# Kernel tuning notes

Measured on AMD Instinct MI355X. Metric: run time of the kernel, lower is better.

## Reference

```python
import jax, jax.numpy as jnp
import numpy as np

N_NODES = 100000
NEG_SLOPE = 0.2
EPS = 1e-16


def gat_conv(x, src, dst, W, a_src, a_dst, b):
    # x: [N, in], W: [in, d]. PyG GATConv with heads=1, concat -> [N, d]
    h = x @ W                                   # [N, d]
    e = jax.nn.leaky_relu((h @ a_src)[src] + (h @ a_dst)[dst], NEG_SLOPE)  # [E]
    # softmax over incoming edges per destination node
    m = jax.ops.segment_max(e, dst, num_segments=N_NODES)   # [N]
    m = jnp.where(jnp.isfinite(m), m, 0.0)
    ex = jnp.exp(e - m[dst])                                 # [E]
    denom = jax.ops.segment_sum(ex, dst, num_segments=N_NODES)
    alpha = ex / (denom[dst] + EPS)                          # [E]
    out = jax.ops.segment_sum(alpha[:, None] * h[src], dst, num_segments=N_NODES)
    return out + b


def setup_inputs() -> dict:
    key = jax.random.key(0)
    ks = jax.random.split(key, 12)
    d_in, d_h = 64, 64
    x = jax.random.normal(ks[0], (N_NODES, d_in), dtype=jnp.float32)
    edge_index = jax.random.randint(ks[1], (2, 1200000), 0, N_NODES, dtype=jnp.int32)
    s = 1.0 / np.sqrt(d_in)
    return {
        "x": x,
        "edge_index": edge_index,
        "W1": jax.random.normal(ks[2], (d_in, d_h), dtype=jnp.float32) * s,
        "a_src1": jax.random.normal(ks[3], (d_h,), dtype=jnp.float32) * s,
        "a_dst1": jax.random.normal(ks[4], (d_h,), dtype=jnp.float32) * s,
        "b1": jnp.zeros((d_h,), dtype=jnp.float32),
        "W2": jax.random.normal(ks[5], (d_h, d_h), dtype=jnp.float32) * s,
        "a_src2": jax.random.normal(ks[6], (d_h,), dtype=jnp.float32) * s,
        "a_dst2": jax.random.normal(ks[7], (d_h,), dtype=jnp.float32) * s,
        "b2": jnp.zeros((d_h,), dtype=jnp.float32),
        "W_out": jax.random.normal(ks[8], (d_h, 1), dtype=jnp.float32) * s,
        "b_out": jnp.zeros((1,), dtype=jnp.float32),
    }


def reference(x, edge_index, W1, a_src1, a_dst1, b1, W2, a_src2, a_dst2, b2, W_out, b_out):
    # PyG GATConv adds self-loops by default
    loop = jnp.arange(N_NODES, dtype=edge_index.dtype)
    src = jnp.concatenate([edge_index[0], loop])
    dst = jnp.concatenate([edge_index[1], loop])
    h = jax.nn.relu(gat_conv(x, src, dst, W1, a_src1, a_dst1, b1))
    h = jax.nn.relu(gat_conv(h, src, dst, W2, a_src2, a_dst2, b2))
    g = jnp.mean(h, axis=0, keepdims=True)   # [1, d]
    return g @ W_out + b_out                  # [1, 1]
```

## Files before the change

kernel.cpp:

```cpp
#include <hip/hip_runtime.h>
#include <math.h>

#define NEG_SLOPE 0.2f
#define EPS 1e-16f
#define PPART 256
#define BMAX 512
#define BSTRIDE 6144
#define GAGG_BLOCKS 2048

__device__ __forceinline__ unsigned short f2bf(float f) {
    unsigned int x = __float_as_uint(f);
    unsigned int r = (x + 0x7FFFu + ((x >> 16) & 1u)) >> 16;
    return (unsigned short)r;
}
__device__ __forceinline__ float bf2f(unsigned short u) {
    return __uint_as_float(((unsigned int)u) << 16);
}

#define XPAD 132
__global__ __launch_bounds__(256) void gemm_hs(
    const float* __restrict__ X, const float* __restrict__ W,
    const float* __restrict__ asrc, const float* __restrict__ adst,
    unsigned short* __restrict__ Hb, float* __restrict__ Ss, float* __restrict__ Sd, int N)
{
    __shared__ float Ws[64 * 64];
    __shared__ float Xs[64 * XPAD];
    int t = threadIdx.x;
    int row0 = blockIdx.x * 128;

    {
        const float4* W4 = (const float4*)W;
        float4* Ws4 = (float4*)Ws;
#pragma unroll
        for (int i = 0; i < 4; ++i) Ws4[i * 256 + t] = W4[i * 256 + t];
    }
    {
        const float4* X4 = (const float4*)X;
#pragma unroll
        for (int i = 0; i < 8; ++i) {
            int v = i * 256 + t;
            int r = v >> 4;
            int c4 = (v & 15) * 4;
            int grow = row0 + r;
            float4 xv = make_float4(0.f, 0.f, 0.f, 0.f);
            if (grow < N) xv = X4[(size_t)grow * 16 + (c4 >> 2)];
            Xs[(c4 + 0) * XPAD + r] = xv.x;
            Xs[(c4 + 1) * XPAD + r] = xv.y;
            Xs[(c4 + 2) * XPAD + r] = xv.z;
            Xs[(c4 + 3) * XPAD + r] = xv.w;
        }
    }
    __syncthreads();

    int cg = t & 7;
    int rg = t >> 3;
    float acc[4][8] = {{0.f}};

#pragma unroll 8
    for (int k = 0; k < 64; ++k) {
        float4 xv = *(const float4*)&Xs[k * XPAD + rg * 4];
        float4 w0 = *(const float4*)&Ws[k * 64 + cg * 8];
        float4 w1 = *(const float4*)&Ws[k * 64 + cg * 8 + 4];
        float xr[4] = {xv.x, xv.y, xv.z, xv.w};
        float wc[8] = {w0.x, w0.y, w0.z, w0.w, w1.x, w1.y, w1.z, w1.w};
#pragma unroll
        for (int r = 0; r < 4; ++r)
#pragma unroll
            for (int c = 0; c < 8; ++c)
                acc[r][c] = fmaf(xr[r], wc[c], acc[r][c]);
    }

    float a_s[8], a_d[8];
#pragma unroll
    for (int j = 0; j < 8; ++j) { a_s[j] = asrc[cg * 8 + j]; a_d[j] = adst[cg * 8 + j]; }
#pragma unroll
    for (int r = 0; r < 4; ++r) {
        int row = row0 + rg * 4 + r;
        float s1 = 0.f, s2 = 0.f;
#pragma unroll
        for (int j = 0; j < 8; ++j) {
            s1 = fmaf(acc[r][j], a_s[j], s1);
            s2 = fmaf(acc[r][j], a_d[j], s2);
        }
#pragma unroll
        for (int off = 1; off < 8; off <<= 1) {
            s1 += __shfl_xor(s1, off);
            s2 += __shfl_xor(s2, off);
        }
        if (row < N) {
            unsigned int p0 = (unsigned int)f2bf(acc[r][0]) | ((unsigned int)f2bf(acc[r][1]) << 16);
            unsigned int p1 = (unsigned int)f2bf(acc[r][2]) | ((unsigned int)f2bf(acc[r][3]) << 16);
            unsigned int p2 = (unsigned int)f2bf(acc[r][4]) | ((unsigned int)f2bf(acc[r][5]) << 16);
            unsigned int p3 = (unsigned int)f2bf(acc[r][6]) | ((unsigned int)f2bf(acc[r][7]) << 16);
            *(uint4*)&Hb[(size_t)row * 64 + cg * 8] = make_uint4(p0, p1, p2, p3);
            if (cg == 0) { Ss[row] = s1; Sd[row] = s2; }
        }
    }
}

__global__ __launch_bounds__(256) void bucket_scatter(
    const int* __restrict__ src, const int* __restrict__ dst,
    int E0, int N, int B, int per,
    int* __restrict__ gcur, int* __restrict__ part)
{
    __shared__ int lh[BMAX];
    __shared__ int gb[BMAX];
    __shared__ int lcur[BMAX];
    int t = threadIdx.x, b = blockIdx.x;
    for (int i = t; i < BMAX; i += 256) lh[i] = 0;
    __syncthreads();
    int Etot = E0 + N;
    int i0 = b * per, i1 = min(Etot, i0 + per);
    for (int i = i0 + t; i < i1; i += 256) {
        int d = (i < E0) ? dst[i] : (i - E0);
        atomicAdd(&lh[d >> 8], 1);
    }
    __syncthreads();
    for (int bin = t; bin < B; bin += 256) {
        int c = lh[bin];
        gb[bin] = c ? atomicAdd(&gcur[bin], c) : 0;
        lcur[bin] = 0;
    }
    __syncthreads();
    for (int i = i0 + t; i < i1; i += 256) {
        int s, d;
        if (i < E0) { s = src[i]; d = dst[i]; } else { s = d = i - E0; }
        int bin = d >> 8;
        int off = atomicAdd(&lcur[bin], 1);
        part[bin * BSTRIDE + gb[bin] + off] = ((d & 255) << 24) | s;
    }
}

__global__ __launch_bounds__(256) void bucket_sort(
    const int* __restrict__ gcur, const int* __restrict__ part,
    int* __restrict__ ptr, int* __restrict__ csr_src,
    int4* __restrict__ smallL, int4* __restrict__ bigL,
    int* __restrict__ nSmall, int* __restrict__ nBig,
    int N, int B, int Etot)
{
    __shared__ int cnts[256];
    __shared__ int sh[256];
    __shared__ int cur[256];
    __shared__ int sBase, bBase, sCnt, bCnt;
    int t = threadIdx.x, bkt = blockIdx.x;

    int v = 0;
    for (int i = t; i < bkt; i += 256) v += gcur[i];
    sh[t] = v;
    __syncthreads();
    for (int off = 128; off; off >>= 1) {
        if (t < off) sh[t] += sh[t + off];
        __syncthreads();
    }
    int base = sh[0];
    int myCnt = gcur[bkt];
    __syncthreads();

    cnts[t] = 0;
    if (t == 0) { sCnt = 0; bCnt = 0; }
    __syncthreads();
    int pbase = bkt * BSTRIDE;
    for (int i = t; i < myCnt; i += 256)
        atomicAdd(&cnts[((unsigned)part[pbase + i]) >> 24], 1);
    __syncthreads();
    sh[t] = cnts[t];
    __syncthreads();
    for (int off = 1; off < 256; off <<= 1) {
        int x = (t >= off) ? sh[t - off] : 0;
        __syncthreads();
        sh[t] += x;
        __syncthreads();
    }
    int lptr = (t > 0) ? sh[t - 1] : 0;
    int node = bkt * 256 + t;
    int deg = cnts[t];
    int p0 = base + lptr;
    if (node < N) ptr[node] = p0;
    if (bkt == 0 && t == 0) ptr[N] = Etot;
    cur[t] = lptr;
    __syncthreads();
    for (int i = t; i < myCnt; i += 256) {
        int p = part[pbase + i];
        int local = ((unsigned)p) >> 24;
        int s = p & 0xFFFFFF;
        int pos = atomicAdd(&cur[local], 1);
        csr_src[base + pos] = s;
    }

    bool isSm = (node < N) && (deg <= 16);
    bool isBg = (node < N) && (deg > 16);
    int myPos = -1;
    if (isSm) myPos = atomicAdd(&sCnt, 1);
    if (isBg) myPos = atomicAdd(&bCnt, 1);
    __syncthreads();
    if (t == 0) {
        sBase = atomicAdd(nSmall, sCnt);
        bBase = atomicAdd(nBig, bCnt);
    }
    __syncthreads();
    if (isSm) smallL[sBase + myPos] = make_int4(node, p0, deg, 0);
    if (isBg) bigL[bBase + myPos] = make_int4(node, p0, deg, 0);
}

__global__ __launch_bounds__(256) void gat_agg_small(
    const int4* __restrict__ lst, const int* __restrict__ nSmallP,
    const int* __restrict__ csr_src,
    const float* __restrict__ Ss, const float* __restrict__ Sd,
    const unsigned short* __restrict__ Hb, const float* __restrict__ bias,
    float* __restrict__ A)
{
    int w = (blockIdx.x * blockDim.x + threadIdx.x) >> 6;
    int lane = threadIdx.x & 63;
    int g = lane >> 4;
    int il = lane & 15;
    int gb = lane & 48;
    int nS = *nSmallP;
    int totWaves = (gridDim.x * blockDim.x) >> 6;
    const ushort4* H4 = (const ushort4*)Hb;
    float4 bv = ((const float4*)bias)[il];

    for (int slot0 = w * 4; slot0 < nS; slot0 += totWaves * 4) {
        int slot = slot0 + g;
        int node = -1, p0 = 0, deg = 0;
        if (slot < nS) { int4 e = lst[slot]; node = e.x; p0 = e.y; deg = e.z; }
        float sdv = (node >= 0) ? Sd[node] : 0.f;
        int s = 0; float e = -INFINITY;
        if (il < deg) {
            s = csr_src[p0 + il];
            float v = Ss[s] + sdv;
            e = (v > 0.f) ? v : NEG_SLOPE * v;
        }
        float m = e;
#pragma unroll
        for (int off = 8; off; off >>= 1) m = fmaxf(m, __shfl_xor(m, off));
        float ex = (il < deg) ? __expf(e - m) : 0.f;
        float den = ex;
#pragma unroll
        for (int off = 8; off; off >>= 1) den += __shfl_xor(den, off);
        float inv = 1.f / (den + EPS);

        float4 acc = make_float4(0.f, 0.f, 0.f, 0.f);
        for (int j = 0; j < deg; ++j) {
            int   sj = __shfl(s, gb + j);
            float aj = __shfl(ex, gb + j);
            ushort4 hv = H4[(size_t)sj * 16 + il];
            acc.x = fmaf(aj, bf2f(hv.x), acc.x);
            acc.y = fmaf(aj, bf2f(hv.y), acc.y);
            acc.z = fmaf(aj, bf2f(hv.z), acc.z);
            acc.w = fmaf(aj, bf2f(hv.w), acc.w);
        }
        if (node >= 0) {
            float4 o;
            o.x = fmaf(acc.x, inv, bv.x); o.x = (o.x > 0.f) ? o.x : 0.f;
            o.y = fmaf(acc.y, inv, bv.y); o.y = (o.y > 0.f) ? o.y : 0.f;
            o.z = fmaf(acc.z, inv, bv.z); o.z = (o.z > 0.f) ? o.z : 0.f;
            o.w = fmaf(acc.w, inv, bv.w); o.w = (o.w > 0.f) ? o.w : 0.f;
            ((float4*)A)[(size_t)node * 16 + il] = o;
        }
    }
}

__global__ __launch_bounds__(256) void gat_agg_big(
    const int4* __restrict__ lst, const int* __restrict__ nBigP,
    const int* __restrict__ csr_src,
    const float* __restrict__ Ss, const float* __restrict__ Sd,
    const unsigned short* __restrict__ Hb, const float* __restrict__ bias,
    float* __restrict__ A)
{
    int w = (blockIdx.x * blockDim.x + threadIdx.x) >> 6;
    int lane = threadIdx.x & 63;
    int nB = *nBigP;
    int totWaves = (gridDim.x * blockDim.x) >> 6;
    int q  = lane >> 4;
    int fl = lane & 15;
    const ushort4* H4 = (const ushort4*)Hb;

    for (int slot = w; slot < nB; slot += totWaves) {
        int4 ent = lst[slot];
        int node = ent.x, p0 = ent.y, deg = ent.z;
        float sdv = Sd[node];
        float4 acc = make_float4(0.f, 0.f, 0.f, 0.f);
        float inv;

        if (deg <= 64) {
            int s = 0; float e = -INFINITY;
            if (lane < deg) {
                s = csr_src[p0 + lane];
                float v = Ss[s] + sdv;
                e = (v > 0.f) ? v : NEG_SLOPE * v;
            }
            float m = e;
#pragma unroll
            for (int off = 32; off; off >>= 1) m = fmaxf(m, __shfl_xor(m, off));
            float ex = (lane < deg) ? __expf(e - m) : 0.f;
            float den = ex;
#pragma unroll
            for (int off = 32; off; off >>= 1) den += __shfl_xor(den, off);
            inv = 1.f / (den + EPS);
            for (int jb = 0; jb < deg; jb += 4) {
                int j = jb + q;
                int   sj = __shfl(s, j);
                float aj = __shfl(ex, j);
                ushort4 hv = H4[(size_t)sj * 16 + fl];
                acc.x = fmaf(aj, bf2f(hv.x), acc.x);
                acc.y = fmaf(aj, bf2f(hv.y), acc.y);
                acc.z = fmaf(aj, bf2f(hv.z), acc.z);
                acc.w = fmaf(aj, bf2f(hv.w), acc.w);
            }
        } else {
            float m = -INFINITY;
            for (int base = 0; base < deg; base += 64) {
                int idx = base + lane;
                float e = -INFINITY;
                if (idx < deg) {
                    int s = csr_src[p0 + idx];
                    float v = Ss[s] + sdv;
                    e = (v > 0.f) ? v : NEG_SLOPE * v;
                }
#pragma unroll
                for (int off = 32; off; off >>= 1) e = fmaxf(e, __shfl_xor(e, off));
                m = fmaxf(m, e);
            }
            float den = 0.f;
            for (int base = 0; base < deg; base += 64) {
                int idx = base + lane;
                float ex = 0.f;
                if (idx < deg) {
                    int s = csr_src[p0 + idx];
                    float v = Ss[s] + sdv;
                    float e = (v > 0.f) ? v : NEG_SLOPE * v;
                    ex = __expf(e - m);
                }
#pragma unroll
                for (int off = 32; off; off >>= 1) ex += __shfl_xor(ex, off);
                den += ex;
            }
            inv = 1.f / (den + EPS);
            for (int base = 0; base < deg; base += 64) {
                int idx = base + lane;
                int s = 0; float ex = 0.f;
                if (idx < deg) {
                    s = csr_src[p0 + idx];
                    float v = Ss[s] + sdv;
                    float e = (v > 0.f) ? v : NEG_SLOPE * v;
                    ex = __expf(e - m);
                }
                int cnt = min(64, deg - base);
                for (int jb = 0; jb < cnt; jb += 4) {
                    int j = jb + q;
                    int   sj = __shfl(s, j);
                    float aj = __shfl(ex, j);
                    ushort4 hv = H4[(size_t)sj * 16 + fl];
                    acc.x = fmaf(aj, bf2f(hv.x), acc.x);
                    acc.y = fmaf(aj, bf2f(hv.y), acc.y);
                    acc.z = fmaf(aj, bf2f(hv.z), acc.z);
                    acc.w = fmaf(aj, bf2f(hv.w), acc.w);
                }
            }
        }

#pragma unroll
        for (int off = 16; off < 64; off <<= 1) {
            acc.x += __shfl_xor(acc.x, off);
            acc.y += __shfl_xor(acc.y, off);
            acc.z += __shfl_xor(acc.z, off);
            acc.w += __shfl_xor(acc.w, off);
        }
        if (q == 0) {
            float4 bv = ((const float4*)bias)[fl];
            float4 o;
            o.x = fmaf(acc.x, inv, bv.x); o.x = (o.x > 0.f) ? o.x : 0.f;
            o.y = fmaf(acc.y, inv, bv.y); o.y = (o.y > 0.f) ? o.y : 0.f;
            o.z = fmaf(acc.z, inv, bv.z); o.z = (o.z > 0.f) ? o.z : 0.f;
            o.w = fmaf(acc.w, inv, bv.w); o.w = (o.w > 0.f) ? o.w : 0.f;
            ((float4*)A)[(size_t)node * 16 + fl] = o;
        }
    }
}

__global__ __launch_bounds__(256) void colsum(const float* __restrict__ A, int total,
                                              float* __restrict__ G)
{
    __shared__ float red[256];
    int t = threadIdx.x;
    int idx = blockIdx.x * blockDim.x + t;
    int stride = gridDim.x * blockDim.x;
    float acc = 0.f;
    for (int i = idx; i < total; i += stride) acc += A[i];
    red[t] = acc;
    __syncthreads();
    if (t < 64) {
        float s = red[t] + red[t + 64] + red[t + 128] + red[t + 192];
        unsafeAtomicAdd(&G[t], s);
    }
}

__global__ void final_out(const float* __restrict__ G, const float* __restrict__ Wout,
                          const float* __restrict__ bout, float* __restrict__ out, float invN)
{
    int lane = threadIdx.x;
    float v = G[lane] * invN * Wout[lane];
#pragma unroll
    for (int off = 32; off; off >>= 1) v += __shfl_down(v, off);
    if (lane == 0) out[0] = v + bout[0];
}

extern "C" void kernel_launch(void* const* d_in, const int* in_sizes, int n_in,
                              void* d_out, int out_size, void* d_ws, size_t ws_size,
                              hipStream_t stream)
{
    const float* x    = (const float*)d_in[0];
    const int*   ei   = (const int*)d_in[1];
    const float* W1   = (const float*)d_in[2];
    const float* as1  = (const float*)d_in[3];
    const float* ad1  = (const float*)d_in[4];
    const float* b1   = (const float*)d_in[5];
    const float* W2   = (const float*)d_in[6];
    const float* as2  = (const float*)d_in[7];
    const float* ad2  = (const float*)d_in[8];
    const float* b2   = (const float*)d_in[9];
    const float* Wout = (const float*)d_in[10];
    const float* bout = (const float*)d_in[11];
    float* out = (float*)d_out;

    int N    = in_sizes[0] / 64;
    int E0   = in_sizes[1] / 2;
    int Etot = E0 + N;
    const int* srcp = ei;
    const int* dstp = ei + E0;

    int B   = (N + 255) >> 8;
    int per = (Etot + PPART - 1) / PPART;

    unsigned short* Hb = (unsigned short*)d_ws;
    float* A   = (float*)d_ws + (size_t)N * 32;
    float* Ss  = A + (size_t)N * 64;
    float* Sd  = Ss + N;
    float* G   = Sd + N;
    int* ptr   = (int*)(G + 64);
    int* gcur  = ptr + N + 1;
    int* nSmall = gcur + 512;
    int* nBig   = nSmall + 1;
    int* part  = nBig + 1;
    int* csr_src = part + (size_t)B * BSTRIDE;
    int4* smallL = (int4*)(csr_src + Etot);
    int4* bigL   = smallL + N;

    int gGemm = (N + 127) / 128;

    hipMemsetAsync(gcur, 0, (512 + 2) * sizeof(int), stream);
    bucket_scatter<<<PPART, 256, 0, stream>>>(srcp, dstp, E0, N, B, per, gcur, part);
    bucket_sort<<<B, 256, 0, stream>>>(gcur, part, ptr, csr_src, smallL, bigL,
                                       nSmall, nBig, N, B, Etot);

    gemm_hs<<<gGemm, 256, 0, stream>>>(x, W1, as1, ad1, Hb, Ss, Sd, N);
    gat_agg_small<<<GAGG_BLOCKS, 256, 0, stream>>>(smallL, nSmall, csr_src, Ss, Sd, Hb, b1, A);
    gat_agg_big<<<GAGG_BLOCKS, 256, 0, stream>>>(bigL, nBig, csr_src, Ss, Sd, Hb, b1, A);

    gemm_hs<<<gGemm, 256, 0, stream>>>(A, W2, as2, ad2, Hb, Ss, Sd, N);
    gat_agg_small<<<GAGG_BLOCKS, 256, 0, stream>>>(smallL, nSmall, csr_src, Ss, Sd, Hb, b2, A);
    gat_agg_big<<<GAGG_BLOCKS, 256, 0, stream>>>(bigL, nBig, csr_src, Ss, Sd, Hb, b2, A);

    hipMemsetAsync(G, 0, 64 * 4, stream);
    colsum<<<304, 256, 0, stream>>>(A, N * 64, G);
    final_out<<<1, 64, 0, stream>>>(G, Wout, bout, out, 1.0f / (float)N);
}
```

Before: 287.5 us.

## Fuse scatter with first GEMM, merge aggregation kernels, fold readout into layer-2

After: 236.8 us. -17.6%, faster.

```diff
diff --git a/kernel.cpp b/kernel.cpp
--- a/kernel.cpp
+++ b/kernel.cpp
@@ -18,15 +18,15 @@
 }
 
 #define XPAD 132
-__global__ __launch_bounds__(256) void gemm_hs(
+__device__ __forceinline__ void gemm_body(
+    char* smem, int bid, int t,
     const float* __restrict__ X, const float* __restrict__ W,
     const float* __restrict__ asrc, const float* __restrict__ adst,
     unsigned short* __restrict__ Hb, float* __restrict__ Ss, float* __restrict__ Sd, int N)
 {
-    __shared__ float Ws[64 * 64];
-    __shared__ float Xs[64 * XPAD];
-    int t = threadIdx.x;
-    int row0 = blockIdx.x * 128;
+    float* Ws = (float*)smem;
+    float* Xs = Ws + 4096;
+    int row0 = bid * 128;
 
     {
         const float4* W4 = (const float4*)W;
@@ -98,15 +98,15 @@
     }
 }
 
-__global__ __launch_bounds__(256) void bucket_scatter(
+__device__ __forceinline__ void scatter_body(
+    char* smem, int b, int t,
     const int* __restrict__ src, const int* __restrict__ dst,
     int E0, int N, int B, int per,
     int* __restrict__ gcur, int* __restrict__ part)
 {
-    __shared__ int lh[BMAX];
-    __shared__ int gb[BMAX];
-    __shared__ int lcur[BMAX];
-    int t = threadIdx.x, b = blockIdx.x;
+    int* lh   = (int*)smem;
+    int* gb   = lh + BMAX;
+    int* lcur = gb + BMAX;
     for (int i = t; i < BMAX; i += 256) lh[i] = 0;
     __syncthreads();
     int Etot = E0 + N;
@@ -129,6 +129,31 @@
         int off = atomicAdd(&lcur[bin], 1);
         part[bin * BSTRIDE + gb[bin] + off] = ((d & 255) << 24) | s;
     }
+}
+
+__global__ __launch_bounds__(256) void k1_scatter_gemm(
+    const int* __restrict__ src, const int* __restrict__ dst,
+    int E0, int N, int B, int per,
+    int* __restrict__ gcur, int* __restrict__ part,
+    const float* __restrict__ X, const float* __restrict__ W,
+    const float* __restrict__ asrc, const float* __restrict__ adst,
+    unsigned short* __restrict__ Hb, float* __restrict__ Ss, float* __restrict__ Sd)
+{
+    __shared__ char smem[50176];
+    int t = threadIdx.x;
+    if (blockIdx.x < PPART)
+        scatter_body(smem, blockIdx.x, t, src, dst, E0, N, B, per, gcur, part);
+    else
+        gemm_body(smem, blockIdx.x - PPART, t, X, W, asrc, adst, Hb, Ss, Sd, N);
+}
+
+__global__ __launch_bounds__(256) void gemm_hs(
+    const float* __restrict__ X, const float* __restrict__ W,
+    const float* __restrict__ asrc, const float* __restrict__ adst,
+    unsigned short* __restrict__ Hb, float* __restrict__ Ss, float* __restrict__ Sd, int N)
+{
+    __shared__ char smem[50176];
+    gemm_body(smem, blockIdx.x, threadIdx.x, X, W, asrc, adst, Hb, Ss, Sd, N);
 }
 
 __global__ __launch_bounds__(256) void bucket_sort(
@@ -202,151 +227,101 @@
     if (isBg) bigL[bBase + myPos] = make_int4(node, p0, deg, 0);
 }
 
-__global__ __launch_bounds__(256) void gat_agg_small(
-    const int4* __restrict__ lst, const int* __restrict__ nSmallP,
+__global__ __launch_bounds__(256) void gat_agg_fused(
+    const int4* __restrict__ smallL, const int* __restrict__ nSmallP,
+    const int4* __restrict__ bigL, const int* __restrict__ nBigP,
     const int* __restrict__ csr_src,
     const float* __restrict__ Ss, const float* __restrict__ Sd,
     const unsigned short* __restrict__ Hb, const float* __restrict__ bias,
-    float* __restrict__ A)
-{
-    int w = (blockIdx.x * blockDim.x + threadIdx.x) >> 6;
-    int lane = threadIdx.x & 63;
-    int g = lane >> 4;
-    int il = lane & 15;
-    int gb = lane & 48;
-    int nS = *nSmallP;
+    float* __restrict__ A, const float* __restrict__ Wout,
+    float* __restrict__ partials, int mode)
+{
+    __shared__ float red[256];
+    int t = threadIdx.x;
+    int w = (blockIdx.x * blockDim.x + t) >> 6;
+    int lane = t & 63;
     int totWaves = (gridDim.x * blockDim.x) >> 6;
     const ushort4* H4 = (const ushort4*)Hb;
-    float4 bv = ((const float4*)bias)[il];
-
-    for (int slot0 = w * 4; slot0 < nS; slot0 += totWaves * 4) {
-        int slot = slot0 + g;
-        int node = -1, p0 = 0, deg = 0;
-        if (slot < nS) { int4 e = lst[slot]; node = e.x; p0 = e.y; deg = e.z; }
-        float sdv = (node >= 0) ? Sd[node] : 0.f;
-        int s = 0; float e = -INFINITY;
-        if (il < deg) {
-            s = csr_src[p0 + il];
-            float v = Ss[s] + sdv;
-            e = (v > 0.f) ? v : NEG_SLOPE * v;
-        }
-        float m = e;
-#pragma unroll
-        for (int off = 8; off; off >>= 1) m = fmaxf(m, __shfl_xor(m, off));
-        float ex = (il < deg) ? __expf(e - m) : 0.f;
-        float den = ex;
-#pragma unroll
-        for (int off = 8; off; off >>= 1) den += __shfl_xor(den, off);
-        float inv = 1.f / (den + EPS);
-
-        float4 acc = make_float4(0.f, 0.f, 0.f, 0.f);
-        for (int j = 0; j < deg; ++j) {
-            int   sj = __shfl(s, gb + j);
-            float aj = __shfl(ex, gb + j);
-            ushort4 hv = H4[(size_t)sj * 16 + il];
-            acc.x = fmaf(aj, bf2f(hv.x), acc.x);
-            acc.y = fmaf(aj, bf2f(hv.y), acc.y);
-            acc.z = fmaf(aj, bf2f(hv.z), acc.z);
-            acc.w = fmaf(aj, bf2f(hv.w), acc.w);
-        }
-        if (node >= 0) {
-            float4 o;
-            o.x = fmaf(acc.x, inv, bv.x); o.x = (o.x > 0.f) ? o.x : 0.f;
-            o.y = fmaf(acc.y, inv, bv.y); o.y = (o.y > 0.f) ? o.y : 0.f;
-            o.z = fmaf(acc.z, inv, bv.z); o.z = (o.z > 0.f) ? o.z : 0.f;
-            o.w = fmaf(acc.w, inv, bv.w); o.w = (o.w > 0.f) ? o.w : 0.f;
-            ((float4*)A)[(size_t)node * 16 + il] = o;
-        }
-    }
-}
-
-__global__ __launch_bounds__(256) void gat_agg_big(
-    const int4* __restrict__ lst, const int* __restrict__ nBigP,
-    const int* __restrict__ csr_src,
-    const float* __restrict__ Ss, const float* __restrict__ Sd,
-    const unsigned short* __restrict__ Hb, const float* __restrict__ bias,
-    float* __restrict__ A)
-{
-    int w = (blockIdx.x * blockDim.x + threadIdx.x) >> 6;
-    int lane = threadIdx.x & 63;
-    int nB = *nBigP;
-    int totWaves = (gridDim.x * blockDim.x) >> 6;
-    int q  = lane >> 4;
-    int fl = lane & 15;
-    const ushort4* H4 = (const ushort4*)Hb;
-
-    for (int slot = w; slot < nB; slot += totWaves) {
-        int4 ent = lst[slot];
-        int node = ent.x, p0 = ent.y, deg = ent.z;
-        float sdv = Sd[node];
-        float4 acc = make_float4(0.f, 0.f, 0.f, 0.f);
-        float inv;
-
-        if (deg <= 64) {
+    float dsum = 0.f;
+
+    {
+        int g = lane >> 4;
+        int il = lane & 15;
+        int gb = lane & 48;
+        int nS = *nSmallP;
+        float4 bv = ((const float4*)bias)[il];
+        float4 wv = ((const float4*)Wout)[il];
+        for (int slot0 = w * 4; slot0 < nS; slot0 += totWaves * 4) {
+            int slot = slot0 + g;
+            int node = -1, p0 = 0, deg = 0;
+            if (slot < nS) { int4 e = smallL[slot]; node = e.x; p0 = e.y; deg = e.z; }
+            float sdv = (node >= 0) ? Sd[node] : 0.f;
             int s = 0; float e = -INFINITY;
-            if (lane < deg) {
-                s = csr_src[p0 + lane];
-                float v = Ss[s] + sdv;
-                e = (v > 0.f) ? v : NEG_SLOPE * v;
+            if (il < deg) {
+                s = csr_src[p0 + il];
+                float vv = Ss[s] + sdv;
+                e = (vv > 0.f) ? vv : NEG_SLOPE * vv;
             }
             float m = e;
 #pragma unroll
-            for (int off = 32; off; off >>= 1) m = fmaxf(m, __shfl_xor(m, off));
-            float ex = (lane < deg) ? __expf(e - m) : 0.f;
+            for (int off = 8; off; off >>= 1) m = fmaxf(m, __shfl_xor(m, off));
+            float ex = (il < deg) ? __expf(e - m) : 0.f;
             float den = ex;
 #pragma unroll
-            for (int off = 32; off; off >>= 1) den += __shfl_xor(den, off);
-            inv = 1.f / (den + EPS);
-            for (int jb = 0; jb < deg; jb += 4) {
-                int j = jb + q;
-                int   sj = __shfl(s, j);
-                float aj = __shfl(ex, j);
-                ushort4 hv = H4[(size_t)sj * 16 + fl];
+            for (int off = 8; off; off >>= 1) den += __shfl_xor(den, off);
+            float inv = 1.f / (den + EPS);
+
+            float4 acc = make_float4(0.f, 0.f, 0.f, 0.f);
+            for (int j = 0; j < deg; ++j) {
+                int   sj = __shfl(s, gb + j);
+                float aj = __shfl(ex, gb + j);
+                ushort4 hv = H4[(size_t)sj * 16 + il];
                 acc.x = fmaf(aj, bf2f(hv.x), acc.x);
                 acc.y = fmaf(aj, bf2f(hv.y), acc.y);
                 acc.z = fmaf(aj, bf2f(hv.z), acc.z);
                 acc.w = fmaf(aj, bf2f(hv.w), acc.w);
             }
-        } else {
-            float m = -INFINITY;
-            for (int base = 0; base < deg; base += 64) {
-                int idx = base + lane;
-                float e = -INFINITY;
-                if (idx < deg) {
-                    int s = csr_src[p0 + idx];
-                    float v = Ss[s] + sdv;
-                    e = (v > 0.f) ? v : NEG_SLOPE * v;
-                }
-#pragma unroll
-                for (int off = 32; off; off >>= 1) e = fmaxf(e, __shfl_xor(e, off));
-                m = fmaxf(m, e);
-            }
-            float den = 0.f;
-            for (int base = 0; base < deg; base += 64) {
-                int idx = base + lane;
-                float ex = 0.f;
-                if (idx < deg) {
-                    int s = csr_src[p0 + idx];
-                    float v = Ss[s] + sdv;
-                    float e = (v > 0.f) ? v : NEG_SLOPE * v;
-                    ex = __expf(e - m);
-                }
-#pragma unroll
-                for (int off = 32; off; off >>= 1) ex += __shfl_xor(ex, off);
-                den += ex;
-            }
-            inv = 1.f / (den + EPS);
-            for (int base = 0; base < deg; base += 64) {
-                int idx = base + lane;
-                int s = 0; float ex = 0.f;
-                if (idx < deg) {
-                    s = csr_src[p0 + idx];
-                    float v = Ss[s] + sdv;
-                    float e = (v > 0.f) ? v : NEG_SLOPE * v;
-                    ex = __expf(e - m);
-                }
-                int cnt = min(64, deg - base);
-                for (int jb = 0; jb < cnt; jb += 4) {
+            if (node >= 0) {
+                float4 o;
+                o.x = fmaf(acc.x, inv, bv.x); o.x = (o.x > 0.f) ? o.x : 0.f;
+                o.y = fmaf(acc.y, inv, bv.y); o.y = (o.y > 0.f) ? o.y : 0.f;
+                o.z = fmaf(acc.z, inv, bv.z); o.z = (o.z > 0.f) ? o.z : 0.f;
+                o.w = fmaf(acc.w, inv, bv.w); o.w = (o.w > 0.f) ? o.w : 0.f;
+                if (mode == 0)
+                    ((float4*)A)[(size_t)node * 16 + il] = o;
+                else
+                    dsum += o.x * wv.x + o.y * wv.y + o.z * wv.z + o.w * wv.w;
+            }
+        }
+    }
+
+    {
+        int q  = lane >> 4;
+        int fl = lane & 15;
+        int nB = *nBigP;
+        for (int slot = w; slot < nB; slot += totWaves) {
+            int4 ent = bigL[slot];
+            int node = ent.x, p0 = ent.y, deg = ent.z;
+            float sdv = Sd[node];
+            float4 acc = make_float4(0.f, 0.f, 0.f, 0.f);
+            float inv;
+
+            if (deg <= 64) {
+                int s = 0; float e = -INFINITY;
+                if (lane < deg) {
+                    s = csr_src[p0 + lane];
+                    float vv = Ss[s] + sdv;
+                    e = (vv > 0.f) ? vv : NEG_SLOPE * vv;
+                }
+                float m = e;
+#pragma unroll
+                for (int off = 32; off; off >>= 1) m = fmaxf(m, __shfl_xor(m, off));
+                float ex = (lane < deg) ? __expf(e - m) : 0.f;
+                float den = ex;
+#pragma unroll
+                for (int off = 32; off; off >>= 1) den += __shfl_xor(den, off);
+                inv = 1.f / (den + EPS);
+                for (int jb = 0; jb < deg; jb += 4) {
                     int j = jb + q;
                     int   sj = __shfl(s, j);
                     float aj = __shfl(ex, j);
@@ -356,53 +331,108 @@
                     acc.z = fmaf(aj, bf2f(hv.z), acc.z);
                     acc.w = fmaf(aj, bf2f(hv.w), acc.w);
                 }
-            }
-        }
-
-#pragma unroll
-        for (int off = 16; off < 64; off <<= 1) {
-            acc.x += __shfl_xor(acc.x, off);
-            acc.y += __shfl_xor(acc.y, off);
-            acc.z += __shfl_xor(acc.z, off);
-            acc.w += __shfl_xor(acc.w, off);
-        }
-        if (q == 0) {
-            float4 bv = ((const float4*)bias)[fl];
-            float4 o;
-            o.x = fmaf(acc.x, inv, bv.x); o.x = (o.x > 0.f) ? o.x : 0.f;
-            o.y = fmaf(acc.y, inv, bv.y); o.y = (o.y > 0.f) ? o.y : 0.f;
-            o.z = fmaf(acc.z, inv, bv.z); o.z = (o.z > 0.f) ? o.z : 0.f;
-            o.w = fmaf(acc.w, inv, bv.w); o.w = (o.w > 0.f) ? o.w : 0.f;
-            ((float4*)A)[(size_t)node * 16 + fl] = o;
-        }
-    }
-}
-
-__global__ __launch_bounds__(256) void colsum(const float* __restrict__ A, int total,
-                                              float* __restrict__ G)
+            } else {
+                float m = -INFINITY;
+                for (int base = 0; base < deg; base += 64) {
+                    int idx = base + lane;
+                    float e = -INFINITY;
+                    if (idx < deg) {
+                        int s = csr_src[p0 + idx];
+                        float vv = Ss[s] + sdv;
+                        e = (vv > 0.f) ? vv : NEG_SLOPE * vv;
+                    }
+#pragma unroll
+                    for (int off = 32; off; off >>= 1) e = fmaxf(e, __shfl_xor(e, off));
+                    m = fmaxf(m, e);
+                }
+                float den = 0.f;
+                for (int base = 0; base < deg; base += 64) {
+                    int idx = base + lane;
+                    float ex = 0.f;
+                    if (idx < deg) {
+                        int s = csr_src[p0 + idx];
+                        float vv = Ss[s] + sdv;
+                        float e = (vv > 0.f) ? vv : NEG_SLOPE * vv;
+                        ex = __expf(e - m);
+                    }
+#pragma unroll
+                    for (int off = 32; off; off >>= 1) ex += __shfl_xor(ex, off);
+                    den += ex;
+                }
+                inv = 1.f / (den + EPS);
+                for (int base = 0; base < deg; base += 64) {
+                    int idx = base + lane;
+                    int s = 0; float ex = 0.f;
+                    if (idx < deg) {
+                        s = csr_src[p0 + idx];
+                        float vv = Ss[s] + sdv;
+                        float e = (vv > 0.f) ? vv : NEG_SLOPE * vv;
+                        ex = __expf(e - m);
+                    }
+                    int cnt = min(64, deg - base);
+                    for (int jb = 0; jb < cnt; jb += 4) {
+                        int j = jb + q;
+                        int   sj = __shfl(s, j);
+                        float aj = __shfl(ex, j);
+                        ushort4 hv = H4[(size_t)sj * 16 + fl];
+                        acc.x = fmaf(aj, bf2f(hv.x), acc.x);
+                        acc.y = fmaf(aj, bf2f(hv.y), acc.y);
+                        acc.z = fmaf(aj, bf2f(hv.z), acc.z);
+                        acc.w = fmaf(aj, bf2f(hv.w), acc.w);
+                    }
+                }
+            }
+
+#pragma unroll
+            for (int off = 16; off < 64; off <<= 1) {
+                acc.x += __shfl_xor(acc.x, off);
+                acc.y += __shfl_xor(acc.y, off);
+                acc.z += __shfl_xor(acc.z, off);
+                acc.w += __shfl_xor(acc.w, off);
+            }
+            if (q == 0) {
+                float4 bv = ((const float4*)bias)[fl];
+                float4 o;
+                o.x = fmaf(acc.x, inv, bv.x); o.x = (o.x > 0.f) ? o.x : 0.f;
+                o.y = fmaf(acc.y, inv, bv.y); o.y = (o.y > 0.f) ? o.y : 0.f;
+                o.z = fmaf(acc.z, inv, bv.z); o.z = (o.z > 0.f) ? o.z : 0.f;
+                o.w = fmaf(acc.w, inv, bv.w); o.w = (o.w > 0.f) ? o.w : 0.f;
+                if (mode == 0) {
+                    ((float4*)A)[(size_t)node * 16 + fl] = o;
+                } else {
+                    float4 wv = ((const float4*)Wout)[fl];
+                    dsum += o.x * wv.x + o.y * wv.y + o.z * wv.z + o.w * wv.w;
+                }
+            }
+        }
+    }
+
+    if (mode == 1) {
+        red[t] = dsum;
+        __syncthreads();
+        for (int off = 128; off; off >>= 1) {
+            if (t < off) red[t] += red[t + off];
+            __syncthreads();
+        }
+        if (t == 0) partials[blockIdx.x] = red[0];
+    }
+}
+
+__global__ __launch_bounds__(256) void final_reduce(
+    const float* __restrict__ partials, int np,
+    const float* __restrict__ bout, float* __restrict__ out, float invN)
 {
     __shared__ float red[256];
     int t = threadIdx.x;
-    int idx = blockIdx.x * blockDim.x + t;
-    int stride = gridDim.x * blockDim.x;
-    float acc = 0.f;
-    for (int i = idx; i < total; i += stride) acc += A[i];
-    red[t] = acc;
-    __syncthreads();
-    if (t < 64) {
-        float s = red[t] + red[t + 64] + red[t + 128] + red[t + 192];
-        unsafeAtomicAdd(&G[t], s);
-    }
-}
-
-__global__ void final_out(const float* __restrict__ G, const float* __restrict__ Wout,
-                          const float* __restrict__ bout, float* __restrict__ out, float invN)
-{
-    int lane = threadIdx.x;
-    float v = G[lane] * invN * Wout[lane];
-#pragma unroll
-    for (int off = 32; off; off >>= 1) v += __shfl_down(v, off);
-    if (lane == 0) out[0] = v + bout[0];
+    float s = 0.f;
+    for (int i = t; i < np; i += 256) s += partials[i];
+    red[t] = s;
+    __syncthreads();
+    for (int off = 128; off; off >>= 1) {
+        if (t < off) red[t] += red[t + off];
+        __syncthreads();
+    }
+    if (t == 0) out[0] = fmaf(red[0], invN, bout[0]);
 }
 
 extern "C" void kernel_launch(void* const* d_in, const int* in_sizes, int n_in,
@@ -436,8 +466,7 @@
     float* A   = (float*)d_ws + (size_t)N * 32;
     float* Ss  = A + (size_t)N * 64;
     float* Sd  = Ss + N;
-    float* G   = Sd + N;
-    int* ptr   = (int*)(G + 64);
+    int* ptr   = (int*)(Sd + N);
     int* gcur  = ptr + N + 1;
     int* nSmall = gcur + 512;
     int* nBig   = nSmall + 1;
@@ -445,23 +474,26 @@
     int* csr_src = part + (size_t)B * BSTRIDE;
     int4* smallL = (int4*)(csr_src + Etot);
     int4* bigL   = smallL + N;
+    float* partials = (float*)(bigL + N);
 
     int gGemm = (N + 127) / 128;
 
     hipMemsetAsync(gcur, 0, (512 + 2) * sizeof(int), stream);
-    bucket_scatter<<<PPART, 256, 0, stream>>>(srcp, dstp, E0, N, B, per, gcur, part);
+
+    k1_scatter_gemm<<<PPART + gGemm, 256, 0, stream>>>(
+        srcp, dstp, E0, N, B, per, gcur, part,
+        x, W1, as1, ad1, Hb, Ss, Sd);
+
     bucket_sort<<<B, 256, 0, stream>>>(gcur, part, ptr, csr_src, smallL, bigL,
                                        nSmall, nBig, N, B, Etot);
 
-    gemm_hs<<<gGemm, 256, 0, stream>>>(x, W1, as1, ad1, Hb, Ss, Sd, N);
-    gat_agg_small<<<GAGG_BLOCKS, 256, 0, stream>>>(smallL, nSmall, csr_src, Ss, Sd, Hb, b1, A);
-    gat_agg_big<<<GAGG_BLOCKS, 256, 0, stream>>>(bigL, nBig, csr_src, Ss, Sd, Hb, b1, A);
+    gat_agg_fused<<<GAGG_BLOCKS, 256, 0, stream>>>(
+        smallL, nSmall, bigL, nBig, csr_src, Ss, Sd, Hb, b1, A, Wout, partials, 0);
 
     gemm_hs<<<gGemm, 256, 0, stream>>>(A, W2, as2, ad2, Hb, Ss, Sd, N);
-    gat_agg_small<<<GAGG_BLOCKS, 256, 0, stream>>>(smallL, nSmall, csr_src, Ss, Sd, Hb, b2, A);
-    gat_agg_big<<<GAGG_BLOCKS, 256, 0, stream>>>(bigL, nBig, csr_src, Ss, Sd, Hb, b2, A);
-
-    hipMemsetAsync(G, 0, 64 * 4, stream);
-    colsum<<<304, 256, 0, stream>>>(A, N * 64, G);
-    final_out<<<1, 64, 0, stream>>>(G, Wout, bout, out, 1.0f / (float)N);
-}
+
+    gat_agg_fused<<<GAGG_BLOCKS, 256, 0, stream>>>(
+        smallL, nSmall, bigL, nBig, csr_src, Ss, Sd, Hb, b2, A, Wout, partials, 1);
+
+    final_reduce<<<1, 256, 0, stream>>>(partials, GAGG_BLOCKS, bout, out, 1.0f / (float)N);
+}
```
